# Kernel optimization log

Hardware: AMD Instinct MI355X
Metric: run time of the kernel (lower is better)

## Reference

```python
import jax, jax.numpy as jnp
import numpy as np
from jax import lax

B, H, W, C = 8, 128, 128, 192
NUM_HEADS = 4
EPS = 1e-12  # tf.nn.l2_normalize epsilon


def _l2_normalize(x, axis=-1):
    sq = jnp.sum(x * x, axis=axis, keepdims=True)
    return x * lax.rsqrt(jnp.maximum(sq, EPS))


def setup_inputs() -> dict:
    key = jax.random.key(0)
    k1, k2, k3, k4 = jax.random.split(key, 4)
    x = jax.random.normal(k1, (B, H, W, C), dtype=jnp.float32)
    # 1x1 conv -> stored as [C, 3C] matrix
    qkv_w = jax.random.normal(k2, (C, 3 * C), dtype=jnp.float32) * 0.05
    # depthwise 3x3 conv, groups = 3C: HWIO kernel with I=1, O=3C
    dw_w = jax.random.normal(k3, (3, 3, 1, 3 * C), dtype=jnp.float32) * 0.05
    # 1x1 projection conv -> [C, C]
    proj_w = jax.random.normal(k4, (C, C), dtype=jnp.float32) * 0.05
    temperature = jnp.ones((NUM_HEADS, 1, 1), dtype=jnp.float32)
    return {"x": x, "qkv_w": qkv_w, "dw_w": dw_w, "proj_w": proj_w,
            "temperature": temperature}


def reference(x, qkv_w, dw_w, proj_w, temperature):
    b, h, w, c = x.shape
    heads = NUM_HEADS
    c_head = c // heads
    hw = h * w

    # 1x1 conv (no bias)
    qkv = jnp.einsum('bhwc,cd->bhwd', x, qkv_w)  # [b,h,w,3c]
    # depthwise 3x3 conv, SAME padding, groups = 3c
    qkv = lax.conv_general_dilated(
        qkv, dw_w, window_strides=(1, 1), padding='SAME',
        dimension_numbers=('NHWC', 'HWIO', 'NHWC'),
        feature_group_count=3 * c)

    q, k, v = jnp.split(qkv, 3, axis=-1)  # each [b,h,w,c]
    # faithful raw row-major reshape as in the TF code
    q = q.reshape(b, heads, c_head, hw)
    k = k.reshape(b, heads, c_head, hw)
    v = v.reshape(b, heads, c_head, hw)

    q = _l2_normalize(q, axis=-1)
    k = _l2_normalize(k, axis=-1)

    # channel-wise (transposed) attention: [b,heads,c_head,c_head]
    attn = jnp.einsum('bncs,bnds->bncd', q, k)
    attn = attn * temperature[None]  # temperature: [heads,1,1]
    attn = jax.nn.softmax(attn, axis=-1)

    out = jnp.einsum('bncd,bnds->bncs', attn, v)  # [b,heads,c_head,hw]
    out = out.reshape(b, h, w, c)
    out = jnp.einsum('bhwc,cd->bhwd', out, proj_w)  # 1x1 projection
    return out
```

## Files before the change

kernel.cpp:

```cpp
#include <hip/hip_runtime.h>
#include <math.h>

#define HWP 16384
#define CIN 192
#define C3  576
#define CH  48
#define NHD 4
#define NS  64
#define PBF 3145728
#define QKPAD 68
#define KG  192

typedef unsigned short u16;
typedef __attribute__((ext_vector_type(8))) short bf16x8;
typedef __attribute__((ext_vector_type(4))) float f32x4;

__device__ __forceinline__ u16 f2bf(float f) {
  unsigned int u = __builtin_bit_cast(unsigned int, f);
  u = (u + 0x7FFFu + ((u >> 16) & 1u)) >> 16;
  return (u16)u;
}
__device__ __forceinline__ float bflo(unsigned int u) {
  return __builtin_bit_cast(float, u << 16);
}
__device__ __forceinline__ float bfhi(unsigned int u) {
  return __builtin_bit_cast(float, u & 0xFFFF0000u);
}
__device__ __forceinline__ unsigned pk2(float a, float b) {
  return (unsigned)f2bf(a) | ((unsigned)f2bf(b) << 16);
}

__global__ __launch_bounds__(256) void convert_x_k(
    const float* __restrict__ in, u16* __restrict__ out) {
  size_t base = ((size_t)blockIdx.x * 256 + threadIdx.x) * 8;
  float4 a = *(const float4*)&in[base];
  float4 b = *(const float4*)&in[base + 4];
  uint4 o;
  o.x = pk2(a.x, a.y); o.y = pk2(a.z, a.w);
  o.z = pk2(b.x, b.y); o.w = pk2(b.z, b.w);
  *(uint4*)&out[base] = o;
}

__global__ __launch_bounds__(256) void convert_w_k(
    const float* __restrict__ qkvW, const float* __restrict__ projW,
    u16* __restrict__ qkvWT, u16* __restrict__ projWT) {
  int idx = blockIdx.x * 256 + threadIdx.x;
  if (idx < C3 * CIN) {
    int n = idx / CIN, k = idx % CIN;
    qkvWT[idx] = f2bf(qkvW[(size_t)k * C3 + n]);
  } else {
    int i2 = idx - C3 * CIN;
    if (i2 < CIN * CIN) {
      int n = i2 / CIN, k = i2 % CIN;
      projWT[i2] = f2bf(projW[(size_t)k * CIN + n]);
    }
  }
}

template <bool C_BF16>
__global__ __launch_bounds__(256) void gemm1(
    const u16* __restrict__ A, const u16* __restrict__ BT, void* __restrict__ Cv,
    int N) {
  __shared__ __align__(16) u16 As[128 * KG];
  __shared__ __align__(16) u16 Bs[64 * KG];
  const int t = threadIdx.x;
  const int lane = t & 63, wave = t >> 6;
  const int nT = N >> 6;
  const int nwg = gridDim.x;
  const int bid = blockIdx.x;
  const int q = nwg >> 3, r = nwg & 7;
  const int xcd = bid & 7, idx = bid >> 3;
  const int swz = (xcd < r) ? (xcd * (q + 1) + idx)
                            : (r * (q + 1) + (xcd - r) * q + idx);
  const int m0 = (swz / nT) * 128, n0 = (swz % nT) * 64;
  const int wm = (wave >> 1) * 64, wn = (wave & 1) * 32;

  uint4 va[12], vb[6];
#pragma unroll
  for (int i = 0; i < 12; ++i) {
    int slot = t + i * 256;
    int row = slot / 24, c = slot % 24;
    va[i] = *(const uint4*)&A[(size_t)(m0 + row) * KG + c * 8];
  }
#pragma unroll
  for (int i = 0; i < 6; ++i) {
    int slot = t + i * 256;
    int row = slot / 24, c = slot % 24;
    vb[i] = *(const uint4*)&BT[(size_t)(n0 + row) * KG + c * 8];
  }
#pragma unroll
  for (int i = 0; i < 12; ++i) {
    int slot = t + i * 256;
    int row = slot / 24, cb = (slot % 24) * 16;
    *(uint4*)((char*)As + row * 384 + (cb ^ ((row & 7) << 4))) = va[i];
  }
#pragma unroll
  for (int i = 0; i < 6; ++i) {
    int slot = t + i * 256;
    int row = slot / 24, cb = (slot % 24) * 16;
    *(uint4*)((char*)Bs + row * 384 + (cb ^ ((row & 7) << 4))) = vb[i];
  }
  __syncthreads();

  f32x4 acc[4][2];
#pragma unroll
  for (int mi = 0; mi < 4; ++mi)
#pragma unroll
    for (int ni = 0; ni < 2; ++ni) acc[mi][ni] = (f32x4){0.f, 0.f, 0.f, 0.f};

  const int lrow = lane & 15;
  const int lg16 = (lane >> 4) * 16;
#pragma unroll
  for (int kk = 0; kk < 6; ++kk) {
    const int colb = kk * 64 + lg16;
    bf16x8 a[4], b[2];
#pragma unroll
    for (int mi = 0; mi < 4; ++mi) {
      int row = wm + mi * 16 + lrow;
      a[mi] = *(const bf16x8*)((char*)As + row * 384 + (colb ^ ((row & 7) << 4)));
    }
#pragma unroll
    for (int ni = 0; ni < 2; ++ni) {
      int row = wn + ni * 16 + lrow;
      b[ni] = *(const bf16x8*)((char*)Bs + row * 384 + (colb ^ ((row & 7) << 4)));
    }
#pragma unroll
    for (int mi = 0; mi < 4; ++mi)
#pragma unroll
      for (int ni = 0; ni < 2; ++ni)
        acc[mi][ni] = __builtin_amdgcn_mfma_f32_16x16x32_bf16(a[mi], b[ni], acc[mi][ni], 0, 0, 0);
  }

  const int crow = (lane >> 4) * 4, ccol = lane & 15;
#pragma unroll
  for (int mi = 0; mi < 4; ++mi)
#pragma unroll
    for (int ni = 0; ni < 2; ++ni)
#pragma unroll
      for (int rr = 0; rr < 4; ++rr) {
        size_t off = (size_t)(m0 + wm + mi * 16 + crow + rr) * N + n0 + wn + ni * 16 + ccol;
        if (C_BF16) ((u16*)Cv)[off] = f2bf(acc[mi][ni][rr]);
        else        ((float*)Cv)[off] = acc[mi][ni][rr];
      }
}

__global__ __launch_bounds__(192) void dwconv_k(
    const u16* __restrict__ pre, const float* __restrict__ dwW,
    u16* __restrict__ qb, u16* __restrict__ kb, u16* __restrict__ vb,
    float* __restrict__ psum, int b0) {
  __shared__ __align__(16) u16 lds[2400 * 8];
  const int t = threadIdx.x;
  const int tile = blockIdx.x, sel = blockIdx.y, brel = blockIdx.z;
  const int h0 = (tile >> 4) * 8, w0 = (tile & 15) * 8;
  const int cg = t % 24, tw = t / 24;
  const int c = sel * 192 + cg * 8;

  float wgt[9][8];
#pragma unroll
  for (int tap = 0; tap < 9; ++tap) {
    float4 a = *(const float4*)&dwW[(size_t)tap * C3 + c];
    float4 b = *(const float4*)&dwW[(size_t)tap * C3 + c + 4];
    wgt[tap][0] = a.x; wgt[tap][1] = a.y; wgt[tap][2] = a.z; wgt[tap][3] = a.w;
    wgt[tap][4] = b.x; wgt[tap][5] = b.y; wgt[tap][6] = b.z; wgt[tap][7] = b.w;
  }

  const u16* src = pre + (size_t)brel * HWP * C3;
#pragma unroll
  for (int r = 0; r < 13; ++r) {
    int slot = t + r * 192;
    if (slot < 2400) {
      int pix = r * 8 + tw;
      int py = pix / 10, px = pix % 10;
      int gh = h0 - 1 + py, gw = w0 - 1 + px;
      uint4 v = make_uint4(0, 0, 0, 0);
      if ((unsigned)gh < 128u && (unsigned)gw < 128u)
        v = *(const uint4*)&src[(size_t)((gh << 7) + gw) * C3 + c];
      *(uint4*)&lds[slot * 8] = v;
    }
  }
  __syncthreads();

  float ssum[8] = {};
  u16* dstb = (sel == 0 ? qb : sel == 1 ? kb : vb) + (size_t)brel * PBF;
#pragma unroll
  for (int r = 0; r < 8; ++r) {
    float acc[8] = {};
#pragma unroll
    for (int dy = 0; dy < 3; ++dy)
#pragma unroll
      for (int dx = 0; dx < 3; ++dx) {
        uint4 v = *(const uint4*)&lds[(((r + dy) * 10 + tw + dx) * 24 + cg) * 8];
        const float* wg = wgt[dy * 3 + dx];
        acc[0] += bflo(v.x) * wg[0]; acc[1] += bfhi(v.x) * wg[1];
        acc[2] += bflo(v.y) * wg[2]; acc[3] += bfhi(v.y) * wg[3];
        acc[4] += bflo(v.z) * wg[4]; acc[5] += bfhi(v.z) * wg[5];
        acc[6] += bflo(v.w) * wg[6]; acc[7] += bfhi(v.w) * wg[7];
      }
    uint4 o;
    o.x = pk2(acc[0], acc[1]); o.y = pk2(acc[2], acc[3]);
    o.z = pk2(acc[4], acc[5]); o.w = pk2(acc[6], acc[7]);
    *(uint4*)&dstb[(size_t)(((h0 + r) << 7) + w0 + tw) * CIN + cg * 8] = o;
    if (sel < 2) {
#pragma unroll
      for (int i = 0; i < 8; ++i) ssum[i] += acc[i] * acc[i];
    }
  }

  if (sel < 2) {
    __syncthreads();
    float* fl = (float*)lds;
#pragma unroll
    for (int i = 0; i < 8; ++i) fl[tw * 192 + cg * 8 + i] = ssum[i];
    __syncthreads();
    float s = 0.f;
#pragma unroll
    for (int tw2 = 0; tw2 < 8; ++tw2) s += fl[tw2 * 192 + t];
    psum[(((size_t)sel * 8 + (b0 + brel)) * 192 + t) * 256 + tile] = s;
  }
}

__global__ __launch_bounds__(192) void rownorm2_k(
    const float* __restrict__ psum, float* __restrict__ rq, float* __restrict__ rk,
    int b0) {
  int sel = blockIdx.x, brel = blockIdx.y;
  int b = b0 + brel;
  int t = threadIdx.x;
  const float* p = psum + (((size_t)sel * 8 + b) * 192 + t) * 256;
  float s = 0.f;
#pragma unroll 4
  for (int i = 0; i < 256; i += 4) {
    float4 v = *(const float4*)&p[i];
    s += v.x + v.y + v.z + v.w;
  }
  (sel ? rk : rq)[b * CIN + t] = rsqrtf(fmaxf(s, 1e-12f));
}

__global__ __launch_bounds__(256) void qk_partial_k(
    const u16* __restrict__ qbuf, const u16* __restrict__ kbuf,
    float* __restrict__ partial, int b0) {
  int sc = blockIdx.x, n = blockIdx.y, brel = blockIdx.z;
  int b = b0 + brel;
  __shared__ float qs[48][QKPAD];
  __shared__ float ks[48][QKPAD];
  const u16* qp = qbuf + (size_t)brel * PBF + (size_t)n * CH * HWP;
  const u16* kp = kbuf + (size_t)brel * PBF + (size_t)n * CH * HWP;
  int t = threadIdx.x;
  int i0 = (t >> 4) * 3, j0 = (t & 15) * 3;
  float acc[3][3] = {};
  int sBeg = sc * 256;
  for (int s0 = sBeg; s0 < sBeg + 256; s0 += 64) {
    uint2 qv[3], kv[3];
#pragma unroll
    for (int rep = 0; rep < 3; ++rep) {
      int fi = t + rep * 256;
      int row = fi >> 4;
      int sv = (fi & 15) * 4;
      qv[rep] = *(const uint2*)&qp[(size_t)row * HWP + s0 + sv];
      kv[rep] = *(const uint2*)&kp[(size_t)row * HWP + s0 + sv];
    }
    __syncthreads();
#pragma unroll
    for (int rep = 0; rep < 3; ++rep) {
      int fi = t + rep * 256;
      int row = fi >> 4;
      int sv = (fi & 15) * 4;
      qs[row][sv + 0] = bflo(qv[rep].x); qs[row][sv + 1] = bfhi(qv[rep].x);
      qs[row][sv + 2] = bflo(qv[rep].y); qs[row][sv + 3] = bfhi(qv[rep].y);
      ks[row][sv + 0] = bflo(kv[rep].x); ks[row][sv + 1] = bfhi(kv[rep].x);
      ks[row][sv + 2] = bflo(kv[rep].y); ks[row][sv + 3] = bfhi(kv[rep].y);
    }
    __syncthreads();
#pragma unroll
    for (int s4 = 0; s4 < 16; ++s4) {
      float4 q0 = *(const float4*)&qs[i0 + 0][s4 * 4];
      float4 q1 = *(const float4*)&qs[i0 + 1][s4 * 4];
      float4 q2 = *(const float4*)&qs[i0 + 2][s4 * 4];
      float4 k0 = *(const float4*)&ks[j0 + 0][s4 * 4];
      float4 k1 = *(const float4*)&ks[j0 + 1][s4 * 4];
      float4 k2 = *(const float4*)&ks[j0 + 2][s4 * 4];
      acc[0][0] += q0.x*k0.x + q0.y*k0.y + q0.z*k0.z + q0.w*k0.w;
      acc[0][1] += q0.x*k1.x + q0.y*k1.y + q0.z*k1.z + q0.w*k1.w;
      acc[0][2] += q0.x*k2.x + q0.y*k2.y + q0.z*k2.z + q0.w*k2.w;
      acc[1][0] += q1.x*k0.x + q1.y*k0.y + q1.z*k0.z + q1.w*k0.w;
      acc[1][1] += q1.x*k1.x + q1.y*k1.y + q1.z*k1.z + q1.w*k1.w;
      acc[1][2] += q1.x*k2.x + q1.y*k2.y + q1.z*k2.z + q1.w*k2.w;
      acc[2][0] += q2.x*k0.x + q2.y*k0.y + q2.z*k0.z + q2.w*k0.w;
      acc[2][1] += q2.x*k1.x + q2.y*k1.y + q2.z*k1.z + q2.w*k1.w;
      acc[2][2] += q2.x*k2.x + q2.y*k2.y + q2.z*k2.z + q2.w*k2.w;
    }
    __syncthreads();
  }
#pragma unroll
  for (int ii = 0; ii < 3; ++ii)
#pragma unroll
    for (int jj = 0; jj < 3; ++jj)
      partial[((((size_t)b * NHD + n) * NS + sc) * CH + (i0 + ii)) * CH + (j0 + jj)] = acc[ii][jj];
}

__global__ __launch_bounds__(64) void softmax_k(
    const float* __restrict__ partial, const float* __restrict__ rq, const float* __restrict__ rk,
    const float* __restrict__ temp, float* __restrict__ attn, int b0) {
  int i = blockIdx.x % CH;
  int n = (blockIdx.x / CH) % NHD;
  int brel = blockIdx.x / (CH * NHD);
  int b = b0 + brel;
  int j = threadIdx.x;
  float logit = -INFINITY;
  if (j < CH) {
    float s = 0.f;
#pragma unroll 8
    for (int sc = 0; sc < NS; ++sc)
      s += partial[((((size_t)b * NHD + n) * NS + sc) * CH + i) * CH + j];
    logit = s * rq[b * CIN + n * CH + i] * rk[b * CIN + n * CH + j] * temp[n];
  }
  float m = logit;
#pragma unroll
  for (int o = 32; o > 0; o >>= 1) m = fmaxf(m, __shfl_xor(m, o));
  float e = (j < CH) ? expf(logit - m) : 0.f;
  float sum = e;
#pragma unroll
  for (int o = 32; o > 0; o >>= 1) sum += __shfl_xor(sum, o);
  if (j < CH) attn[(((size_t)b * NHD + n) * CH + i) * CH + j] = e / sum;
}

__global__ __launch_bounds__(256) void av_k(
    const float* __restrict__ attn, const u16* __restrict__ vbuf,
    u16* __restrict__ obuf, int b0) {
  int st = blockIdx.x, n = blockIdx.y, brel = blockIdx.z;
  int b = b0 + brel;
  __shared__ float as_[CH * CH];
  int t = threadIdx.x;
  const float* ap = attn + ((size_t)b * NHD + n) * CH * CH;
#pragma unroll
  for (int r = 0; r < 9; ++r) as_[t + r * 256] = ap[t + r * 256];
  __syncthreads();
  int s = st * 512 + t * 2;
  const u16* vp = vbuf + (size_t)brel * PBF + (size_t)n * CH * HWP;
  float2 acc[CH];
#pragma unroll
  for (int d = 0; d < CH; ++d) { acc[d].x = 0.f; acc[d].y = 0.f; }
#pragma unroll 4
  for (int j4 = 0; j4 < 12; ++j4) {
    unsigned int u0 = *(const unsigned int*)&vp[(size_t)(j4 * 4 + 0) * HWP + s];
    unsigned int u1 = *(const unsigned int*)&vp[(size_t)(j4 * 4 + 1) * HWP + s];
    unsigned int u2 = *(const unsigned int*)&vp[(size_t)(j4 * 4 + 2) * HWP + s];
    unsigned int u3 = *(const unsigned int*)&vp[(size_t)(j4 * 4 + 3) * HWP + s];
    float2 v0 = make_float2(bflo(u0), bfhi(u0));
    float2 v1 = make_float2(bflo(u1), bfhi(u1));
    float2 v2 = make_float2(bflo(u2), bfhi(u2));
    float2 v3 = make_float2(bflo(u3), bfhi(u3));
#pragma unroll
    for (int d = 0; d < CH; ++d) {
      float4 a4 = *(const float4*)&as_[d * CH + j4 * 4];
      acc[d].x += a4.x * v0.x + a4.y * v1.x + a4.z * v2.x + a4.w * v3.x;
      acc[d].y += a4.x * v0.y + a4.y * v1.y + a4.z * v2.y + a4.w * v3.y;
    }
  }
  u16* op = obuf + (size_t)brel * PBF + (size_t)n * CH * HWP;
#pragma unroll
  for (int d = 0; d < CH; ++d) {
    ushort2 o; o.x = f2bf(acc[d].x); o.y = f2bf(acc[d].y);
    *(ushort2*)&op[(size_t)d * HWP + s] = o;
  }
}

extern "C" void kernel_launch(void* const* d_in, const int* in_sizes, int n_in,
                              void* d_out, int out_size, void* d_ws, size_t ws_size,
                              hipStream_t stream) {
  const float* x      = (const float*)d_in[0];
  const float* qkv_w  = (const float*)d_in[1];
  const float* dw_w   = (const float*)d_in[2];
  const float* proj_w = (const float*)d_in[3];
  const float* temp   = (const float*)d_in[4];
  float* out = (float*)d_out;

  float* rq      = (float*)d_ws;
  float* rk      = rq + 8 * CIN;
  float* attn    = rk + 8 * CIN;
  float* partial = attn + 8 * NHD * CH * CH;
  float* psum    = partial + (size_t)8 * NHD * NS * CH * CH;
  u16* qkvwT  = (u16*)(psum + (size_t)2 * 8 * 192 * 256);
  u16* projwT = qkvwT + (size_t)C3 * CIN;
  u16* xbf    = projwT + (size_t)CIN * CIN;
  char* bufbase = (char*)(xbf + (size_t)8 * HWP * CIN);
  size_t off = (size_t)(bufbase - (char*)d_ws);
  off = (off + 255) & ~(size_t)255;

  const size_t perBatchBytes = (size_t)HWP * C3 * 2 + 4 * (size_t)PBF * 2;
  size_t avail = ws_size > off ? ws_size - off : 0;
  int nb = (int)(avail / perBatchBytes);
  if (nb < 1) nb = 1;
  if (nb > 8) nb = 8;

  u16* qkv_pre = (u16*)((char*)d_ws + off);
  u16* qbuf = qkv_pre + (size_t)nb * HWP * C3;
  u16* kbuf = qbuf + (size_t)nb * PBF;
  u16* vbuf = kbuf + (size_t)nb * PBF;
  u16* obuf = vbuf + (size_t)nb * PBF;

  convert_x_k<<<dim3((8 * HWP * CIN) / 2048), 256, 0, stream>>>(x, xbf);
  convert_w_k<<<dim3((C3 * CIN + CIN * CIN + 255) / 256), 256, 0, stream>>>(
      qkv_w, proj_w, qkvwT, projwT);

  for (int b0 = 0; b0 < 8; b0 += nb) {
    int nbc = (8 - b0) < nb ? (8 - b0) : nb;
    int M = nbc * HWP;
    gemm1<true><<<dim3((M / 128) * (C3 / 64)), 256, 0, stream>>>(
        xbf + (size_t)b0 * HWP * CIN, qkvwT, qkv_pre, C3);
    dwconv_k<<<dim3(256, 3, nbc), 192, 0, stream>>>(
        qkv_pre, dw_w, qbuf, kbuf, vbuf, psum, b0);
    rownorm2_k<<<dim3(2, nbc), 192, 0, stream>>>(psum, rq, rk, b0);
    qk_partial_k<<<dim3(NS, NHD, nbc), 256, 0, stream>>>(qbuf, kbuf, partial, b0);
    softmax_k<<<dim3(nbc * NHD * CH), 64, 0, stream>>>(partial, rq, rk, temp, attn, b0);
    av_k<<<dim3(HWP / 512, NHD, nbc), 256, 0, stream>>>(attn, vbuf, obuf, b0);
    gemm1<false><<<dim3((M / 128) * (CIN / 64)), 256, 0, stream>>>(
        obuf, projwT, out + (size_t)b0 * HWP * CIN, CIN);
  }
}
```

Measured before the change: 411.4 us.

## Fuse x bf16 conversion into GEMM load and use MFMA for QK^T partials

Drops the separate kernel that converted x to bf16. The first GEMM now reads fp32 x directly and packs it to bf16 while loading, which avoids writing and re-reading a bf16 copy of x. The scalar LDS-based QK^T partial kernel is replaced by a one-wave kernel that uses 16x16x32 bf16 MFMA, reading straight from global memory with 32 spatial chunks instead of 64. The launch grid becomes smaller (NS*4*nb blocks of 64 threads) and the global loads are strided, so occupancy and latency hiding may suffer.

```diff
diff --git a/kernel.cpp b/kernel.cpp
--- a/kernel.cpp
+++ b/kernel.cpp
@@ -6,9 +6,8 @@
 #define C3  576
 #define CH  48
 #define NHD 4
-#define NS  64
+#define NS  32
 #define PBF 3145728
-#define QKPAD 68
 #define KG  192
 
 typedef unsigned short u16;
@@ -28,17 +27,6 @@
 }
 __device__ __forceinline__ unsigned pk2(float a, float b) {
   return (unsigned)f2bf(a) | ((unsigned)f2bf(b) << 16);
-}
-
-__global__ __launch_bounds__(256) void convert_x_k(
-    const float* __restrict__ in, u16* __restrict__ out) {
-  size_t base = ((size_t)blockIdx.x * 256 + threadIdx.x) * 8;
-  float4 a = *(const float4*)&in[base];
-  float4 b = *(const float4*)&in[base + 4];
-  uint4 o;
-  o.x = pk2(a.x, a.y); o.y = pk2(a.z, a.w);
-  o.z = pk2(b.x, b.y); o.w = pk2(b.z, b.w);
-  *(uint4*)&out[base] = o;
 }
 
 __global__ __launch_bounds__(256) void convert_w_k(
@@ -57,9 +45,9 @@
   }
 }
 
-template <bool C_BF16>
+template <bool A_F32, bool C_BF16>
 __global__ __launch_bounds__(256) void gemm1(
-    const u16* __restrict__ A, const u16* __restrict__ BT, void* __restrict__ Cv,
+    const void* __restrict__ Av, const u16* __restrict__ BT, void* __restrict__ Cv,
     int N) {
   __shared__ __align__(16) u16 As[128 * KG];
   __shared__ __align__(16) u16 Bs[64 * KG];
@@ -80,7 +68,15 @@
   for (int i = 0; i < 12; ++i) {
     int slot = t + i * 256;
     int row = slot / 24, c = slot % 24;
-    va[i] = *(const uint4*)&A[(size_t)(m0 + row) * KG + c * 8];
+    if (A_F32) {
+      const float* p = (const float*)Av + (size_t)(m0 + row) * KG + c * 8;
+      float4 f0 = *(const float4*)p;
+      float4 f1 = *(const float4*)(p + 4);
+      va[i].x = pk2(f0.x, f0.y); va[i].y = pk2(f0.z, f0.w);
+      va[i].z = pk2(f1.x, f1.y); va[i].w = pk2(f1.z, f1.w);
+    } else {
+      va[i] = *(const uint4*)((const u16*)Av + (size_t)(m0 + row) * KG + c * 8);
+    }
   }
 #pragma unroll
   for (int i = 0; i < 6; ++i) {
@@ -235,66 +231,49 @@
   (sel ? rk : rq)[b * CIN + t] = rsqrtf(fmaxf(s, 1e-12f));
 }
 
-__global__ __launch_bounds__(256) void qk_partial_k(
+__global__ __launch_bounds__(64) void qk_mfma_k(
     const u16* __restrict__ qbuf, const u16* __restrict__ kbuf,
     float* __restrict__ partial, int b0) {
   int sc = blockIdx.x, n = blockIdx.y, brel = blockIdx.z;
   int b = b0 + brel;
-  __shared__ float qs[48][QKPAD];
-  __shared__ float ks[48][QKPAD];
+  const int lane = threadIdx.x;
   const u16* qp = qbuf + (size_t)brel * PBF + (size_t)n * CH * HWP;
   const u16* kp = kbuf + (size_t)brel * PBF + (size_t)n * CH * HWP;
-  int t = threadIdx.x;
-  int i0 = (t >> 4) * 3, j0 = (t & 15) * 3;
-  float acc[3][3] = {};
-  int sBeg = sc * 256;
-  for (int s0 = sBeg; s0 < sBeg + 256; s0 += 64) {
-    uint2 qv[3], kv[3];
-#pragma unroll
-    for (int rep = 0; rep < 3; ++rep) {
-      int fi = t + rep * 256;
-      int row = fi >> 4;
-      int sv = (fi & 15) * 4;
-      qv[rep] = *(const uint2*)&qp[(size_t)row * HWP + s0 + sv];
-      kv[rep] = *(const uint2*)&kp[(size_t)row * HWP + s0 + sv];
-    }
-    __syncthreads();
-#pragma unroll
-    for (int rep = 0; rep < 3; ++rep) {
-      int fi = t + rep * 256;
-      int row = fi >> 4;
-      int sv = (fi & 15) * 4;
-      qs[row][sv + 0] = bflo(qv[rep].x); qs[row][sv + 1] = bfhi(qv[rep].x);
-      qs[row][sv + 2] = bflo(qv[rep].y); qs[row][sv + 3] = bfhi(qv[rep].y);
-      ks[row][sv + 0] = bflo(kv[rep].x); ks[row][sv + 1] = bfhi(kv[rep].x);
-      ks[row][sv + 2] = bflo(kv[rep].y); ks[row][sv + 3] = bfhi(kv[rep].y);
-    }
-    __syncthreads();
-#pragma unroll
-    for (int s4 = 0; s4 < 16; ++s4) {
-      float4 q0 = *(const float4*)&qs[i0 + 0][s4 * 4];
-      float4 q1 = *(const float4*)&qs[i0 + 1][s4 * 4];
-      float4 q2 = *(const float4*)&qs[i0 + 2][s4 * 4];
-      float4 k0 = *(const float4*)&ks[j0 + 0][s4 * 4];
-      float4 k1 = *(const float4*)&ks[j0 + 1][s4 * 4];
-      float4 k2 = *(const float4*)&ks[j0 + 2][s4 * 4];
-      acc[0][0] += q0.x*k0.x + q0.y*k0.y + q0.z*k0.z + q0.w*k0.w;
-      acc[0][1] += q0.x*k1.x + q0.y*k1.y + q0.z*k1.z + q0.w*k1.w;
-      acc[0][2] += q0.x*k2.x + q0.y*k2.y + q0.z*k2.z + q0.w*k2.w;
-      acc[1][0] += q1.x*k0.x + q1.y*k0.y + q1.z*k0.z + q1.w*k0.w;
-      acc[1][1] += q1.x*k1.x + q1.y*k1.y + q1.z*k1.z + q1.w*k1.w;
-      acc[1][2] += q1.x*k2.x + q1.y*k2.y + q1.z*k2.z + q1.w*k2.w;
-      acc[2][0] += q2.x*k0.x + q2.y*k0.y + q2.z*k0.z + q2.w*k0.w;
-      acc[2][1] += q2.x*k1.x + q2.y*k1.y + q2.z*k1.z + q2.w*k1.w;
-      acc[2][2] += q2.x*k2.x + q2.y*k2.y + q2.z*k2.z + q2.w*k2.w;
-    }
-    __syncthreads();
-  }
-#pragma unroll
-  for (int ii = 0; ii < 3; ++ii)
-#pragma unroll
-    for (int jj = 0; jj < 3; ++jj)
-      partial[((((size_t)b * NHD + n) * NS + sc) * CH + (i0 + ii)) * CH + (j0 + jj)] = acc[ii][jj];
+  const int lrow = lane & 15;
+  const int lko = (lane >> 4) * 8;
+  f32x4 acc[3][3];
+#pragma unroll
+  for (int mi = 0; mi < 3; ++mi)
+#pragma unroll
+    for (int nj = 0; nj < 3; ++nj) acc[mi][nj] = (f32x4){0.f, 0.f, 0.f, 0.f};
+
+  const int sBeg = sc * 512;
+#pragma unroll 4
+  for (int kk = 0; kk < 16; ++kk) {
+    const int s0 = sBeg + kk * 32 + lko;
+    bf16x8 a[3], bb[3];
+#pragma unroll
+    for (int mi = 0; mi < 3; ++mi)
+      a[mi] = *(const bf16x8*)&qp[(size_t)(mi * 16 + lrow) * HWP + s0];
+#pragma unroll
+    for (int nj = 0; nj < 3; ++nj)
+      bb[nj] = *(const bf16x8*)&kp[(size_t)(nj * 16 + lrow) * HWP + s0];
+#pragma unroll
+    for (int mi = 0; mi < 3; ++mi)
+#pragma unroll
+      for (int nj = 0; nj < 3; ++nj)
+        acc[mi][nj] = __builtin_amdgcn_mfma_f32_16x16x32_bf16(a[mi], bb[nj], acc[mi][nj], 0, 0, 0);
+  }
+
+  const int crow = (lane >> 4) * 4, ccol = lane & 15;
+  float* pout = partial + (((size_t)b * NHD + n) * NS + sc) * CH * CH;
+#pragma unroll
+  for (int mi = 0; mi < 3; ++mi)
+#pragma unroll
+    for (int nj = 0; nj < 3; ++nj)
+#pragma unroll
+      for (int rr = 0; rr < 4; ++rr)
+        pout[(size_t)(mi * 16 + crow + rr) * CH + nj * 16 + ccol] = acc[mi][nj][rr];
 }
 
 __global__ __launch_bounds__(64) void softmax_k(
@@ -381,8 +360,7 @@
   float* psum    = partial + (size_t)8 * NHD * NS * CH * CH;
   u16* qkvwT  = (u16*)(psum + (size_t)2 * 8 * 192 * 256);
   u16* projwT = qkvwT + (size_t)C3 * CIN;
-  u16* xbf    = projwT + (size_t)CIN * CIN;
-  char* bufbase = (char*)(xbf + (size_t)8 * HWP * CIN);
+  char* bufbase = (char*)(projwT + (size_t)CIN * CIN);
   size_t off = (size_t)(bufbase - (char*)d_ws);
   off = (off + 255) & ~(size_t)255;
 
@@ -398,22 +376,21 @@
   u16* vbuf = kbuf + (size_t)nb * PBF;
   u16* obuf = vbuf + (size_t)nb * PBF;
 
-  convert_x_k<<<dim3((8 * HWP * CIN) / 2048), 256, 0, stream>>>(x, xbf);
   convert_w_k<<<dim3((C3 * CIN + CIN * CIN + 255) / 256), 256, 0, stream>>>(
       qkv_w, proj_w, qkvwT, projwT);
 
   for (int b0 = 0; b0 < 8; b0 += nb) {
     int nbc = (8 - b0) < nb ? (8 - b0) : nb;
     int M = nbc * HWP;
-    gemm1<true><<<dim3((M / 128) * (C3 / 64)), 256, 0, stream>>>(
-        xbf + (size_t)b0 * HWP * CIN, qkvwT, qkv_pre, C3);
+    gemm1<true, true><<<dim3((M / 128) * (C3 / 64)), 256, 0, stream>>>(
+        x + (size_t)b0 * HWP * CIN, qkvwT, qkv_pre, C3);
     dwconv_k<<<dim3(256, 3, nbc), 192, 0, stream>>>(
         qkv_pre, dw_w, qbuf, kbuf, vbuf, psum, b0);
     rownorm2_k<<<dim3(2, nbc), 192, 0, stream>>>(psum, rq, rk, b0);
-    qk_partial_k<<<dim3(NS, NHD, nbc), 256, 0, stream>>>(qbuf, kbuf, partial, b0);
+    qk_mfma_k<<<dim3(NS, NHD, nbc), 64, 0, stream>>>(qbuf, kbuf, partial, b0);
     softmax_k<<<dim3(nbc * NHD * CH), 64, 0, stream>>>(partial, rq, rk, temp, attn, b0);
     av_k<<<dim3(HWP / 512, NHD, nbc), 256, 0, stream>>>(attn, vbuf, obuf, b0);
-    gemm1<false><<<dim3((M / 128) * (CIN / 64)), 256, 0, stream>>>(
+    gemm1<false, false><<<dim3((M / 128) * (CIN / 64)), 256, 0, stream>>>(
         obuf, projwT, out + (size_t)b0 * HWP * CIN, CIN);
   }
 }
```

Result: faster. 355.6 us (-13.6%).
